# Performance work log

Hardware: AMD Instinct MI355X
Metric: run time of the kernel (lower is better)

## Reference

```python
import jax, jax.numpy as jnp
import numpy as np

D_MODEL = 1024
N_HEADS = 16
HEAD_DIM = D_MODEL // N_HEADS
D_FF = 4096
SEQ = 2048
BATCH = 4
THETA = 10000.0
EPS = 1e-5


def rmsnorm(x, w, eps=EPS):
    xf = x.astype(jnp.float32)
    var = jnp.mean(xf * xf, axis=-1, keepdims=True) + eps
    return (xf * jax.lax.rsqrt(var) * w).astype(x.dtype)


def rope_tables(head_dim, max_len, theta):
    freqs = 1.0 / theta ** (jnp.arange(0, head_dim, 2, dtype=jnp.float32) / head_dim)
    t = jnp.arange(max_len, dtype=jnp.float32)
    ang = jnp.outer(t, freqs)  # [T, Hs/2]
    return jnp.cos(ang), jnp.sin(ang)


def apply_rope(x, cos, sin):
    # x: [B, H, T, Hs]; cos/sin: [T, Hs/2] (broadcast over B, H)
    x1 = x[..., 0::2]
    x2 = x[..., 1::2]
    o1 = x1 * cos - x2 * sin
    o2 = x1 * sin + x2 * cos
    return jnp.stack([o1, o2], axis=-1).reshape(x.shape).astype(x.dtype)


def setup_inputs() -> dict:
    key = jax.random.key(0)
    ks = jax.random.split(key, 12)
    s = 0.02
    return {
        "x": jax.random.normal(ks[0], (BATCH, SEQ, D_MODEL), dtype=jnp.float32),
        "token_positions": jnp.arange(SEQ, dtype=jnp.int32),
        "ln1_w": jnp.ones((D_MODEL,), dtype=jnp.float32),
        "q_w": jax.random.normal(ks[1], (D_MODEL, D_MODEL), dtype=jnp.float32) * s,
        "k_w": jax.random.normal(ks[2], (D_MODEL, D_MODEL), dtype=jnp.float32) * s,
        "v_w": jax.random.normal(ks[3], (D_MODEL, D_MODEL), dtype=jnp.float32) * s,
        "o_w": jax.random.normal(ks[4], (D_MODEL, D_MODEL), dtype=jnp.float32) * s,
        "ln2_w": jnp.ones((D_MODEL,), dtype=jnp.float32),
        "w1": jax.random.normal(ks[5], (D_FF, D_MODEL), dtype=jnp.float32) * s,
        "w2": jax.random.normal(ks[6], (D_MODEL, D_FF), dtype=jnp.float32) * s,
        "w3": jax.random.normal(ks[7], (D_FF, D_MODEL), dtype=jnp.float32) * s,
    }


def reference(x, token_positions, ln1_w, q_w, k_w, v_w, o_w, ln2_w, w1, w2, w3):
    B, T, D = x.shape
    cos_full, sin_full = rope_tables(HEAD_DIM, SEQ, THETA)
    cos = cos_full[token_positions]
    sin = sin_full[token_positions]

    # --- attention sublayer ---
    h = rmsnorm(x, ln1_w)
    q = jnp.einsum('btd,od->bto', h, q_w)
    k = jnp.einsum('btd,od->bto', h, k_w)
    v = jnp.einsum('btd,od->bto', h, v_w)
    # [B, T, D] -> [B, H, T, Hs]
    def split_heads(t_):
        return t_.reshape(B, T, N_HEADS, HEAD_DIM).transpose(0, 2, 1, 3)
    xq, xk, xv = split_heads(q), split_heads(k), split_heads(v)
    xq = apply_rope(xq, cos, sin)
    xk = apply_rope(xk, cos, sin)

    scores = jnp.einsum('bhqd,bhkd->bhqk', xq, xk) / jnp.sqrt(jnp.float32(HEAD_DIM))
    causal = jnp.tril(jnp.ones((T, T), dtype=bool))
    scores = jnp.where(causal, scores, jnp.float32(-jnp.inf))
    attn = jax.nn.softmax(scores, axis=-1)
    ctx = jnp.einsum('bhqk,bhkd->bhqd', attn, xv)
    ctx = ctx.transpose(0, 2, 1, 3).reshape(B, T, D)
    x = x + jnp.einsum('btd,od->bto', ctx, o_w)

    # --- SwiGLU FFN sublayer ---
    h2 = rmsnorm(x, ln2_w)
    a = jnp.einsum('btd,fd->btf', h2, w1)
    g = jnp.einsum('btd,fd->btf', h2, w3)
    ff = jnp.einsum('btf,df->btd', a * jax.nn.sigmoid(a) * g, w2)
    return x + ff
```

## Files before the change

### kernel.cpp

```cpp
#include <hip/hip_runtime.h>
#include <hip/hip_bf16.h>

#define D_MODEL 1024
#define N_HEADS 16
#define HEAD_DIM 64
#define D_FF 4096
#define SEQ 2048
#define BATCH 4
#define NTOK (BATCH*SEQ)
#define QS 3072

typedef __attribute__((ext_vector_type(4))) float  f32x4;
typedef __attribute__((ext_vector_type(8))) short  s16x8;
typedef __attribute__((ext_vector_type(4))) unsigned short u16x4;

typedef __attribute__((address_space(1))) const unsigned int gas_u32;
typedef __attribute__((address_space(3))) unsigned int las_u32;

__device__ __forceinline__ void gload_lds16(const void* g, void* l) {
  __builtin_amdgcn_global_load_lds((gas_u32*)g, (las_u32*)l, 16, 0, 0);
}

__device__ __forceinline__ float bf2f(unsigned short u) {
  union { unsigned int i; float f; } v; v.i = ((unsigned int)u) << 16; return v.f;
}
__device__ __forceinline__ unsigned short f2bf(float f) {
  union { float f; unsigned int i; } v; v.f = f;
  return (unsigned short)((v.i + 0x7fffu + ((v.i >> 16) & 1u)) >> 16);
}

__global__ __launch_bounds__(256) void cvt_all_k(const float* __restrict__ qw, const float* __restrict__ kw,
                                                 const float* __restrict__ vw, const float* __restrict__ ow,
                                                 const float* __restrict__ w1, const float* __restrict__ w2,
                                                 const float* __restrict__ w3,
                                                 unsigned short* __restrict__ wqkv, unsigned short* __restrict__ wo,
                                                 unsigned short* __restrict__ b1, unsigned short* __restrict__ b2,
                                                 unsigned short* __restrict__ b3) {
  const long MM = 1 << 20;
  long e = ((long)blockIdx.x*256 + threadIdx.x)*4;
  const float* src; unsigned short* dst; long off;
  if      (e <    MM) { src = qw; dst = wqkv;        off = e; }
  else if (e <  2*MM) { src = kw; dst = wqkv + MM;   off = e - MM; }
  else if (e <  3*MM) { src = vw; dst = wqkv + 2*MM; off = e - 2*MM; }
  else if (e <  4*MM) { src = ow; dst = wo;          off = e - 3*MM; }
  else if (e <  8*MM) { src = w1; dst = b1;          off = e - 4*MM; }
  else if (e < 12*MM) { src = w2; dst = b2;          off = e - 8*MM; }
  else                { src = w3; dst = b3;          off = e - 12*MM; }
  f32x4 v = *(const f32x4*)&src[off];
  u16x4 o;
  #pragma unroll
  for (int c=0;c<4;c++) o[c] = f2bf(v[c]);
  *(u16x4*)&dst[off] = o;
}

__global__ __launch_bounds__(256) void rope_tables_k(const int* __restrict__ pos,
                                                     float* __restrict__ cosT,
                                                     float* __restrict__ sinT) {
  int idx = blockIdx.x*256 + threadIdx.x;
  int t = idx >> 5, i = idx & 31;
  float p  = (float)pos[t];
  float fr = powf(10000.0f, -(float)i * (1.0f/32.0f));
  float ang = p * fr;
  cosT[idx] = cosf(ang);
  sinT[idx] = sinf(ang);
}

__global__ __launch_bounds__(256) void rmsnorm_k(const float* __restrict__ x,
                                                 const float* __restrict__ wgt,
                                                 unsigned short* __restrict__ out) {
  const long row = blockIdx.x;
  const int t = threadIdx.x;
  f32x4 v = *(const f32x4*)&x[row*D_MODEL + t*4];
  float ss = v[0]*v[0] + v[1]*v[1] + v[2]*v[2] + v[3]*v[3];
  #pragma unroll
  for (int off=1; off<64; off<<=1) ss += __shfl_xor(ss, off, 64);
  __shared__ float red[4];
  if ((t & 63) == 0) red[t >> 6] = ss;
  __syncthreads();
  float tot = red[0] + red[1] + red[2] + red[3];
  float inv = rsqrtf(tot * (1.0f/D_MODEL) + 1e-5f);
  f32x4 wv = *(const f32x4*)&wgt[t*4];
  u16x4 o;
  #pragma unroll
  for (int c=0;c<4;c++) o[c] = f2bf(v[c] * inv * wv[c]);
  *(u16x4*)&out[row*D_MODEL + t*4] = o;
}

__global__ __launch_bounds__(256) void rope_k(unsigned short* __restrict__ qkv,
                                              const float* __restrict__ cosT,
                                              const float* __restrict__ sinT) {
  long idx = (long)blockIdx.x*256 + threadIdx.x;
  int ig = (int)(idx & 7);
  long th = idx >> 3;
  int h = (int)(th & 15);
  long bt = th >> 4;
  int t = (int)(bt & (SEQ-1));
  long off = bt*QS + h*HEAD_DIM + ig*8;
  f32x4 cs = *(const f32x4*)&cosT[t*32 + ig*4];
  f32x4 sn = *(const f32x4*)&sinT[t*32 + ig*4];
  s16x8 qv = *(const s16x8*)&qkv[off];
  s16x8 kv = *(const s16x8*)&qkv[off + 1024];
  s16x8 qo, ko;
  #pragma unroll
  for (int p=0;p<4;p++) {
    float q1 = bf2f((unsigned short)qv[2*p]), q2 = bf2f((unsigned short)qv[2*p+1]);
    qo[2*p]   = (short)f2bf((q1*cs[p] - q2*sn[p]) * 0.125f);
    qo[2*p+1] = (short)f2bf((q1*sn[p] + q2*cs[p]) * 0.125f);
    float k1 = bf2f((unsigned short)kv[2*p]), k2 = bf2f((unsigned short)kv[2*p+1]);
    ko[2*p]   = (short)f2bf(k1*cs[p] - k2*sn[p]);
    ko[2*p+1] = (short)f2bf(k1*sn[p] + k2*cs[p]);
  }
  *(s16x8*)&qkv[off] = qo;
  *(s16x8*)&qkv[off + 1024] = ko;
}

template<int EPI>
__global__ __launch_bounds__(512, 2) void gemm8p(const unsigned short* __restrict__ A,
                                                 const unsigned short* __restrict__ W,
                                                 unsigned short* __restrict__ Cb,
                                                 float* __restrict__ Cf,
                                                 const float* __restrict__ resid,
                                                 int M, int N, int K) {
  __shared__ __align__(16) unsigned short As[3][256*64];
  __shared__ __align__(16) unsigned short Bs[3][128*64];

  const int nwg = gridDim.x * gridDim.y;
  int orig = blockIdx.y * gridDim.x + blockIdx.x;
  int swz = orig;
  if ((nwg & 7) == 0) { int cpx = nwg >> 3; swz = (orig & 7) * cpx + (orig >> 3); }
  const int bx = swz % gridDim.x;
  const int by = swz / gridDim.x;

  const int tid = threadIdx.x;
  const int wid = tid >> 6;
  const int l  = tid & 63;
  const int lr = l & 15;
  const int lg = l >> 4;
  const int wm = (wid >> 2) * 128;
  const int wn = (wid & 3) * 32;

  const long rowA0 = (long)by * 256;
  const long rowB0 = (long)bx * 128;
  const int nk = K >> 6;

  auto stA = [&](int bf, int kt, int it) {
    int chunk = it*512 + tid;
    int row = chunk >> 3;
    int csw = (chunk & 7) ^ (row & 7);
    gload_lds16(&A[(rowA0 + row)*(long)K + kt + csw*8], &As[bf][chunk*8]);
  };
  auto stB = [&](int bf, int kt, int it) {
    int chunk = it*512 + tid;
    int row = chunk >> 3;
    int csw = (chunk & 7) ^ (row & 7);
    gload_lds16(&W[(rowB0 + row)*(long)K + kt + csw*8], &Bs[bf][chunk*8]);
  };

  f32x4 acc[8][2] = {};

  stA(0,0,0); stA(0,0,1); stA(0,0,2); stA(0,0,3); stB(0,0,0); stB(0,0,1);
  stA(1,64,0); stA(1,64,1); stA(1,64,2); stA(1,64,3); stB(1,64,0); stB(1,64,1);
  asm volatile("s_waitcnt vmcnt(6)" ::: "memory");
  __builtin_amdgcn_s_barrier();

  int buf = 0;
  for (int ki = 0; ki < nk; ++ki) {
    const int sb = (buf >= 1) ? buf - 1 : buf + 2;
    const int kt2 = (ki + 2) << 6;
    const bool st = (ki + 2) < nk;

    s16x8 af[2][4], bfr[2][2];
    #pragma unroll
    for (int m=0;m<4;m++) {
      int r = wm + m*16 + lr;
      #pragma unroll
      for (int kk=0;kk<2;kk++)
        af[kk][m] = *(const s16x8*)&As[buf][r*64 + ((kk*4+lg)^(r&7))*8];
    }
    #pragma unroll
    for (int n=0;n<2;n++) {
      int r = wn + n*16 + lr;
      #pragma unroll
      for (int kk=0;kk<2;kk++)
        bfr[kk][n] = *(const s16x8*)&Bs[buf][r*64 + ((kk*4+lg)^(r&7))*8];
    }
    if (st) { stA(sb,kt2,0); stA(sb,kt2,1); stB(sb,kt2,0); }
    __builtin_amdgcn_s_barrier();
    __builtin_amdgcn_s_setprio(1);
    #pragma unroll
    for (int kk=0;kk<2;kk++)
      #pragma unroll
      for (int m=0;m<4;m++)
        #pragma unroll
        for (int n=0;n<2;n++)
          acc[m][n] = __builtin_amdgcn_mfma_f32_16x16x32_bf16(af[kk][m], bfr[kk][n], acc[m][n], 0,0,0);
    __builtin_amdgcn_s_setprio(0);
    __builtin_amdgcn_s_barrier();

    #pragma unroll
    for (int m=0;m<4;m++) {
      int r = wm + 64 + m*16 + lr;
      #pragma unroll
      for (int kk=0;kk<2;kk++)
        af[kk][m] = *(const s16x8*)&As[buf][r*64 + ((kk*4+lg)^(r&7))*8];
    }
    if (st) { stA(sb,kt2,2); stA(sb,kt2,3); stB(sb,kt2,1); }
    __builtin_amdgcn_s_barrier();
    __builtin_amdgcn_s_setprio(1);
    #pragma unroll
    for (int kk=0;kk<2;kk++)
      #pragma unroll
      for (int m=0;m<4;m++)
        #pragma unroll
        for (int n=0;n<2;n++)
          acc[4+m][n] = __builtin_amdgcn_mfma_f32_16x16x32_bf16(af[kk][m], bfr[kk][n], acc[4+m][n], 0,0,0);
    __builtin_amdgcn_s_setprio(0);
    if (st)             { asm volatile("s_waitcnt vmcnt(6)" ::: "memory"); }
    else if (ki+1 < nk) { asm volatile("s_waitcnt vmcnt(0)" ::: "memory"); }
    __builtin_amdgcn_s_barrier();

    buf = (buf == 2) ? 0 : buf + 1;
  }

  #pragma unroll
  for (int mi=0;mi<8;mi++)
    #pragma unroll
    for (int n=0;n<2;n++)
      #pragma unroll
      for (int rr=0;rr<4;rr++) {
        long row = rowA0 + wm + mi*16 + lg*4 + rr;
        long col = rowB0 + wn + n*16 + lr;
        float val = acc[mi][n][rr];
        if constexpr (EPI == 0) {
          Cb[row*(long)N + col] = f2bf(val);
        } else {
          Cf[row*(long)N + col] = resid[row*(long)N + col] + val;
        }
      }
}

__global__ __launch_bounds__(256) void attn_k(const unsigned short* __restrict__ QKV,
                                              unsigned short* __restrict__ O) {
  const int bh = blockIdx.x;
  const int b = bh >> 4;
  const int h = bh & 15;
  const int tid = threadIdx.x;
  const int w  = tid >> 6;
  const int l  = tid & 63;
  const int lr = l & 15;
  const int lg = l >> 4;

  const unsigned short* Qp = QKV;
  const unsigned short* Kp = QKV + 1024;
  const unsigned short* Vp = QKV + 2048;

  __shared__ __align__(16) unsigned short Ks[2][64*64];
  __shared__ __align__(16) unsigned short Vs[2][64*64];
  __shared__ __align__(16) unsigned short Ps[4][16][64];

  const int skv = tid >> 2;
  const int sd0 = (tid & 3) * 16;
  const long hbase = (long)(b*SEQ)*QS + h*HEAD_DIM;

  for (int pass = 0; pass < 2; ++pass) {
    const int qt = pass ? 31 - (int)blockIdx.y : (int)blockIdx.y;
    const int q0 = qt * 64;
    const int ntile = qt + 1;

    const long rowQ = (long)(b*SEQ + q0 + w*16 + lr);
    s16x8 qf0 = *(const s16x8*)&Qp[rowQ*QS + h*HEAD_DIM + lg*8];
    s16x8 qf1 = *(const s16x8*)&Qp[rowQ*QS + h*HEAD_DIM + 32 + lg*8];

    float mi = -1e30f, li = 0.f;
    f32x4 oa[4] = {};

    #pragma unroll
    for (int it=0; it<2; ++it) {
      int chunk = it*256 + tid;
      int row = chunk >> 3;
      int csw = (chunk & 7) ^ (row & 7);
      gload_lds16(&Kp[hbase + (long)row*QS + csw*8], &Ks[0][chunk*8]);
    }
    {
      const unsigned short* src = &Vp[hbase + (long)skv*QS + sd0];
      s16x8 v0 = *(const s16x8*)&src[0];
      s16x8 v1 = *(const s16x8*)&src[8];
      #pragma unroll
      for (int i=0;i<16;i++) {
        int d = sd0 + i;
        int key = (d&7) ^ ((d>>3)&7);
        int c = (skv>>3) ^ key;
        Vs[0][d*64 + c*8 + (skv&7)] = (unsigned short)(i<8 ? v0[i] : v1[i-8]);
      }
    }
    __syncthreads();

    for (int t=0; t<ntile; ++t) {
      const int kv0 = t*64;
      const int cur = t & 1;
      const int nb  = cur ^ 1;
      const bool more = (t+1 < ntile);

      s16x8 v0, v1;
      if (more) {
        #pragma unroll
        for (int it=0; it<2; ++it) {
          int chunk = it*256 + tid;
          int row = chunk >> 3;
          int csw = (chunk & 7) ^ (row & 7);
          gload_lds16(&Kp[hbase + (long)(kv0 + 64 + row)*QS + csw*8], &Ks[nb][chunk*8]);
        }
        const unsigned short* src = &Vp[hbase + (long)(kv0 + 64 + skv)*QS + sd0];
        v0 = *(const s16x8*)&src[0];
        v1 = *(const s16x8*)&src[8];
      }

      f32x4 s[4];
      __builtin_amdgcn_s_setprio(1);
      #pragma unroll
      for (int j=0;j<4;j++) {
        int krow = j*16 + lr;
        s16x8 kf0 = *(const s16x8*)&Ks[cur][krow*64 + ((lg)     ^ (krow&7))*8];
        s16x8 kf1 = *(const s16x8*)&Ks[cur][krow*64 + ((4 + lg) ^ (krow&7))*8];
        f32x4 acc = {};
        acc = __builtin_amdgcn_mfma_f32_16x16x32_bf16(kf0, qf0, acc, 0,0,0);
        acc = __builtin_amdgcn_mfma_f32_16x16x32_bf16(kf1, qf1, acc, 0,0,0);
        s[j] = acc;
      }
      __builtin_amdgcn_s_setprio(0);

      if (t == ntile-1) {
        #pragma unroll
        for (int j=0;j<4;j++)
          #pragma unroll
          for (int r=0;r<4;r++)
            if (kv0 + j*16 + lg*4 + r > q0 + w*16 + lr) s[j][r] = -1e30f;
      }

      float pmax = s[0][0];
      #pragma unroll
      for (int j=0;j<4;j++)
        #pragma unroll
        for (int r=0;r<4;r++) pmax = fmaxf(pmax, s[j][r]);
      pmax = fmaxf(pmax, __shfl_xor(pmax, 16, 64));
      pmax = fmaxf(pmax, __shfl_xor(pmax, 32, 64));
      float mn = fmaxf(mi, pmax);
      float al = __expf(mi - mn);
      mi = mn;
      float psum = 0.f;
      #pragma unroll
      for (int j=0;j<4;j++)
        #pragma unroll
        for (int r=0;r<4;r++) {
          float p = __expf(s[j][r] - mn);
          s[j][r] = p;
          psum += p;
        }
      psum += __shfl_xor(psum, 16, 64);
      psum += __shfl_xor(psum, 32, 64);
      li = li*al + psum;

      float alq[4];
      #pragma unroll
      for (int r=0;r<4;r++) alq[r] = __shfl(al, lg*4 + r, 64);
      #pragma unroll
      for (int d=0;d<4;d++)
        #pragma unroll
        for (int r=0;r<4;r++) oa[d][r] *= alq[r];

      #pragma unroll
      for (int j=0;j<4;j++)
        #pragma unroll
        for (int r=0;r<4;r++) {
          int k = j*16 + lg*4 + r;
          int pos = ((k>>3) ^ (lr&7))*8 + (k&7);
          Ps[w][lr][pos] = f2bf(s[j][r]);
        }

      if (more) {
        #pragma unroll
        for (int i=0;i<16;i++) {
          int d = sd0 + i;
          int key = (d&7) ^ ((d>>3)&7);
          int c = (skv>>3) ^ key;
          Vs[nb][d*64 + c*8 + (skv&7)] = (unsigned short)(i<8 ? v0[i] : v1[i-8]);
        }
      }

      __builtin_amdgcn_s_setprio(1);
      #pragma unroll
      for (int kk=0;kk<2;kk++) {
        s16x8 pa = *(const s16x8*)&Ps[w][lr][((kk*4 + lg) ^ (lr&7))*8];
        #pragma unroll
        for (int d=0;d<4;d++) {
          int vrow = d*16 + lr;
          int key = (vrow&7) ^ ((vrow>>3)&7);
          int c = (kk*4 + lg) ^ key;
          s16x8 vb = *(const s16x8*)&Vs[cur][vrow*64 + c*8];
          oa[d] = __builtin_amdgcn_mfma_f32_16x16x32_bf16(pa, vb, oa[d], 0,0,0);
        }
      }
      __builtin_amdgcn_s_setprio(0);
      __syncthreads();
    }

    float liq[4];
    #pragma unroll
    for (int r=0;r<4;r++) liq[r] = __shfl(li, lg*4 + r, 64);
    #pragma unroll
    for (int d=0;d<4;d++)
      #pragma unroll
      for (int r=0;r<4;r++) {
        long row = (long)(b*SEQ + q0 + w*16 + lg*4 + r);
        O[row*D_MODEL + h*HEAD_DIM + d*16 + lr] = f2bf(oa[d][r] / liq[r]);
      }
  }
}

__global__ __launch_bounds__(256) void swiglu_k(unsigned short* __restrict__ a,
                                                const unsigned short* __restrict__ g) {
  long i = ((long)blockIdx.x*256 + threadIdx.x)*8;
  s16x8 av = *(const s16x8*)&a[i];
  s16x8 gv = *(const s16x8*)&g[i];
  s16x8 o;
  #pragma unroll
  for (int c=0;c<8;c++) {
    float xx = bf2f((unsigned short)av[c]);
    float yy = bf2f((unsigned short)gv[c]);
    float sg = 1.0f / (1.0f + __expf(-xx));
    o[c] = (short)f2bf(xx * sg * yy);
  }
  *(s16x8*)&a[i] = o;
}

extern "C" void kernel_launch(void* const* d_in, const int* in_sizes, int n_in,
                              void* d_out, int out_size, void* d_ws, size_t ws_size,
                              hipStream_t stream) {
  (void)in_sizes; (void)n_in; (void)out_size; (void)ws_size;
  const float* x    = (const float*)d_in[0];
  const int*   tpos = (const int*)d_in[1];
  const float* ln1  = (const float*)d_in[2];
  const float* qw   = (const float*)d_in[3];
  const float* kw   = (const float*)d_in[4];
  const float* vw   = (const float*)d_in[5];
  const float* ow   = (const float*)d_in[6];
  const float* ln2  = (const float*)d_in[7];
  const float* w1   = (const float*)d_in[8];
  const float* w2   = (const float*)d_in[9];
  const float* w3   = (const float*)d_in[10];
  float* out = (float*)d_out;

  char* ws = (char*)d_ws;
  size_t off = 0;
  auto nalloc = [&](size_t b) { void* p = ws + off; off += (b + 255) & ~(size_t)255; return p; };

  unsigned short* wqkvb = (unsigned short*)nalloc((size_t)3072*D_MODEL*2);
  unsigned short* wob   = (unsigned short*)nalloc((size_t)D_MODEL*D_MODEL*2);
  unsigned short* w1b   = (unsigned short*)nalloc((size_t)D_FF*D_MODEL*2);
  unsigned short* w3b   = (unsigned short*)nalloc((size_t)D_FF*D_MODEL*2);
  unsigned short* w2b   = (unsigned short*)nalloc((size_t)D_MODEL*D_FF*2);
  float* cosT = (float*)nalloc((size_t)SEQ*32*4);
  float* sinT = (float*)nalloc((size_t)SEQ*32*4);
  unsigned short* hbuf = (unsigned short*)nalloc((size_t)NTOK*D_MODEL*2);
  unsigned short* qkv  = (unsigned short*)nalloc((size_t)NTOK*QS*2);
  unsigned short* ctxb = (unsigned short*)nalloc((size_t)NTOK*D_MODEL*2);
  float* x2 = (float*)nalloc((size_t)NTOK*D_MODEL*4);
  unsigned short* gbuf = (unsigned short*)nalloc((size_t)NTOK*D_FF*2);
  unsigned short* abuf = qkv;

  cvt_all_k<<<16384,256,0,stream>>>(qw, kw, vw, ow, w1, w2, w3,
                                    wqkvb, wob, w1b, w2b, w3b);
  rope_tables_k<<<SEQ*32/256,256,0,stream>>>(tpos, cosT, sinT);

  rmsnorm_k<<<NTOK,256,0,stream>>>(x, ln1, hbuf);
  gemm8p<0><<<dim3(24,32),512,0,stream>>>(hbuf, wqkvb, qkv, nullptr, nullptr, NTOK, QS, D_MODEL);
  rope_k<<<4096,256,0,stream>>>(qkv, cosT, sinT);
  attn_k<<<dim3(64,16),256,0,stream>>>(qkv, ctxb);
  gemm8p<1><<<dim3(8,32),512,0,stream>>>(ctxb, wob, nullptr, x2, x, NTOK, D_MODEL, D_MODEL);

  rmsnorm_k<<<NTOK,256,0,stream>>>(x2, ln2, hbuf);
  gemm8p<0><<<dim3(32,32),512,0,stream>>>(hbuf, w1b, abuf, nullptr, nullptr, NTOK, D_FF, D_MODEL);
  gemm8p<0><<<dim3(32,32),512,0,stream>>>(hbuf, w3b, gbuf, nullptr, nullptr, NTOK, D_FF, D_MODEL);
  swiglu_k<<<(long)NTOK*D_FF/8/256,256,0,stream>>>(abuf, gbuf);
  gemm8p<1><<<dim3(8,32),512,0,stream>>>(abuf, w2b, nullptr, out, x2, NTOK, D_MODEL, D_FF);
}
```

Measured before the change: 637.8 us.

## Template GEMM on tile shape, use 256x256 tiles with quadrant-split double buffering

The GEMM kernel becomes a template over block and warp tile shape. It switches from a triple-buffered 256x128 pipeline to a double-buffered one that splits each k-step into four MFMA quadrants, with staggered half-tile global-to-LDS loads between them. The QKV and FFN up/gate GEMMs now use 256x256 tiles, which roughly halves operand reloads per output and gives each warp a 128x64 subtile with more MFMA reuse. The cost is more accumulator registers (128 fp32 per thread) at the 2-blocks-per-CU launch bound, LDS use of 128 KB per block, and fewer workgroups for the same GEMMs.

After: 644.5 us. About the same (+1.0%).

```diff
diff --git a/kernel.cpp b/kernel.cpp
--- a/kernel.cpp
+++ b/kernel.cpp
@@ -114,15 +114,24 @@
   *(s16x8*)&qkv[off + 1024] = ko;
 }
 
-template<int EPI>
+template<int EPI, int BM, int BN, int WR, int WC>
 __global__ __launch_bounds__(512, 2) void gemm8p(const unsigned short* __restrict__ A,
                                                  const unsigned short* __restrict__ W,
                                                  unsigned short* __restrict__ Cb,
                                                  float* __restrict__ Cf,
                                                  const float* __restrict__ resid,
                                                  int M, int N, int K) {
-  __shared__ __align__(16) unsigned short As[3][256*64];
-  __shared__ __align__(16) unsigned short Bs[3][128*64];
+  constexpr int WTM = BM / WR;
+  constexpr int WTN = BN / WC;
+  constexpr int MR  = WTM / 16;
+  constexpr int NR  = WTN / 16;
+  constexpr int M2  = MR / 2, N2 = NR / 2;
+  constexpr int LA  = BM / 128;
+  constexpr int LB  = BN / 128;
+  constexpr int VMC = 2*LA + LB;
+
+  __shared__ __align__(16) unsigned short As[2][BM*64];
+  __shared__ __align__(16) unsigned short Bs[2][BN*64];
 
   const int nwg = gridDim.x * gridDim.y;
   int orig = blockIdx.y * gridDim.x + blockIdx.x;
@@ -136,100 +145,104 @@
   const int l  = tid & 63;
   const int lr = l & 15;
   const int lg = l >> 4;
-  const int wm = (wid >> 2) * 128;
-  const int wn = (wid & 3) * 32;
-
-  const long rowA0 = (long)by * 256;
-  const long rowB0 = (long)bx * 128;
+  const int wr = wid / WC;
+  const int wc = wid % WC;
+
+  const long rowA0 = (long)by * BM;
+  const long rowB0 = (long)bx * BN;
   const int nk = K >> 6;
 
-  auto stA = [&](int bf, int kt, int it) {
-    int chunk = it*512 + tid;
-    int row = chunk >> 3;
-    int csw = (chunk & 7) ^ (row & 7);
-    gload_lds16(&A[(rowA0 + row)*(long)K + kt + csw*8], &As[bf][chunk*8]);
+  auto stA = [&](int b, int kt, int h) {
+    #pragma unroll
+    for (int it = 0; it < LA; ++it) {
+      int c = it*512 + tid;
+      int row = h*(BM/2) + (c >> 3);
+      int csw = (c & 7) ^ (row & 7);
+      gload_lds16(&A[(rowA0 + row)*(long)K + kt + csw*8], &As[b][row*64 + (c&7)*8]);
+    }
   };
-  auto stB = [&](int bf, int kt, int it) {
-    int chunk = it*512 + tid;
-    int row = chunk >> 3;
-    int csw = (chunk & 7) ^ (row & 7);
-    gload_lds16(&W[(rowB0 + row)*(long)K + kt + csw*8], &Bs[bf][chunk*8]);
+  auto stB = [&](int b, int kt, int h) {
+    #pragma unroll
+    for (int it = 0; it < LB; ++it) {
+      int c = it*512 + tid;
+      int row = h*(BN/2) + (c >> 3);
+      int csw = (c & 7) ^ (row & 7);
+      gload_lds16(&W[(rowB0 + row)*(long)K + kt + csw*8], &Bs[b][row*64 + (c&7)*8]);
+    }
   };
 
-  f32x4 acc[8][2] = {};
-
-  stA(0,0,0); stA(0,0,1); stA(0,0,2); stA(0,0,3); stB(0,0,0); stB(0,0,1);
-  stA(1,64,0); stA(1,64,1); stA(1,64,2); stA(1,64,3); stB(1,64,0); stB(1,64,1);
-  asm volatile("s_waitcnt vmcnt(6)" ::: "memory");
+  f32x4 acc[MR][NR] = {};
+  s16x8 afr[MR][2], bfr[NR][2];
+
+  auto ldA = [&](int b, int mh) {
+    #pragma unroll
+    for (int m=0;m<M2;m++) {
+      int row = wr*WTM + (mh*M2+m)*16 + lr;
+      #pragma unroll
+      for (int kk=0;kk<2;kk++)
+        afr[mh*M2+m][kk] = *(const s16x8*)&As[b][row*64 + ((kk*4+lg)^(row&7))*8];
+    }
+  };
+  auto ldB = [&](int b, int nh) {
+    #pragma unroll
+    for (int n=0;n<N2;n++) {
+      int row = wc*WTN + (nh*N2+n)*16 + lr;
+      #pragma unroll
+      for (int kk=0;kk<2;kk++)
+        bfr[nh*N2+n][kk] = *(const s16x8*)&Bs[b][row*64 + ((kk*4+lg)^(row&7))*8];
+    }
+  };
+  auto mm = [&](int mh, int nh) {
+    #pragma unroll
+    for (int kk=0;kk<2;kk++)
+      #pragma unroll
+      for (int m=0;m<M2;m++)
+        #pragma unroll
+        for (int n=0;n<N2;n++)
+          acc[mh*M2+m][nh*N2+n] = __builtin_amdgcn_mfma_f32_16x16x32_bf16(
+              afr[mh*M2+m][kk], bfr[nh*N2+n][kk], acc[mh*M2+m][nh*N2+n], 0,0,0);
+  };
+
+  stA(0,0,0); stA(0,0,1); stB(0,0,0); stB(0,0,1);
+  stA(1,64,0); stA(1,64,1); stB(1,64,0);
+  asm volatile("s_waitcnt vmcnt(%0)" :: "n"(VMC) : "memory");
   __builtin_amdgcn_s_barrier();
 
-  int buf = 0;
-  for (int ki = 0; ki < nk; ++ki) {
-    const int sb = (buf >= 1) ? buf - 1 : buf + 2;
-    const int kt2 = (ki + 2) << 6;
-    const bool st = (ki + 2) < nk;
-
-    s16x8 af[2][4], bfr[2][2];
-    #pragma unroll
-    for (int m=0;m<4;m++) {
-      int r = wm + m*16 + lr;
-      #pragma unroll
-      for (int kk=0;kk<2;kk++)
-        af[kk][m] = *(const s16x8*)&As[buf][r*64 + ((kk*4+lg)^(r&7))*8];
-    }
-    #pragma unroll
-    for (int n=0;n<2;n++) {
-      int r = wn + n*16 + lr;
-      #pragma unroll
-      for (int kk=0;kk<2;kk++)
-        bfr[kk][n] = *(const s16x8*)&Bs[buf][r*64 + ((kk*4+lg)^(r&7))*8];
-    }
-    if (st) { stA(sb,kt2,0); stA(sb,kt2,1); stB(sb,kt2,0); }
-    __builtin_amdgcn_s_barrier();
-    __builtin_amdgcn_s_setprio(1);
-    #pragma unroll
-    for (int kk=0;kk<2;kk++)
-      #pragma unroll
-      for (int m=0;m<4;m++)
-        #pragma unroll
-        for (int n=0;n<2;n++)
-          acc[m][n] = __builtin_amdgcn_mfma_f32_16x16x32_bf16(af[kk][m], bfr[kk][n], acc[m][n], 0,0,0);
-    __builtin_amdgcn_s_setprio(0);
-    __builtin_amdgcn_s_barrier();
-
-    #pragma unroll
-    for (int m=0;m<4;m++) {
-      int r = wm + 64 + m*16 + lr;
-      #pragma unroll
-      for (int kk=0;kk<2;kk++)
-        af[kk][m] = *(const s16x8*)&As[buf][r*64 + ((kk*4+lg)^(r&7))*8];
-    }
-    if (st) { stA(sb,kt2,2); stA(sb,kt2,3); stB(sb,kt2,1); }
-    __builtin_amdgcn_s_barrier();
-    __builtin_amdgcn_s_setprio(1);
-    #pragma unroll
-    for (int kk=0;kk<2;kk++)
-      #pragma unroll
-      for (int m=0;m<4;m++)
-        #pragma unroll
-        for (int n=0;n<2;n++)
-          acc[4+m][n] = __builtin_amdgcn_mfma_f32_16x16x32_bf16(af[kk][m], bfr[kk][n], acc[4+m][n], 0,0,0);
-    __builtin_amdgcn_s_setprio(0);
-    if (st)             { asm volatile("s_waitcnt vmcnt(6)" ::: "memory"); }
-    else if (ki+1 < nk) { asm volatile("s_waitcnt vmcnt(0)" ::: "memory"); }
-    __builtin_amdgcn_s_barrier();
-
-    buf = (buf == 2) ? 0 : buf + 1;
+  int ba = 0;
+  for (int t = 0; t < nk; ++t) {
+    const int kt1 = (t+1) << 6, kt2 = (t+2) << 6;
+    const bool s2 = (t+2) < nk;
+    ldA(ba, 0); ldB(ba, 0);
+    if (t+1 < nk) stB(ba^1, kt1, 1);
+    __builtin_amdgcn_s_barrier();
+    __builtin_amdgcn_s_setprio(1); mm(0,0); __builtin_amdgcn_s_setprio(0);
+    __builtin_amdgcn_s_barrier();
+    ldA(ba, 1); ldB(ba, 1);
+    if (s2) stA(ba, kt2, 0);
+    __builtin_amdgcn_s_barrier();
+    __builtin_amdgcn_s_setprio(1); mm(1,0); __builtin_amdgcn_s_setprio(0);
+    __builtin_amdgcn_s_barrier();
+    if (s2) stA(ba, kt2, 1);
+    __builtin_amdgcn_s_barrier();
+    __builtin_amdgcn_s_setprio(1); mm(0,1); __builtin_amdgcn_s_setprio(0);
+    __builtin_amdgcn_s_barrier();
+    if (s2) stB(ba, kt2, 0);
+    __builtin_amdgcn_s_barrier();
+    __builtin_amdgcn_s_setprio(1); mm(1,1); __builtin_amdgcn_s_setprio(0);
+    if (s2)             { asm volatile("s_waitcnt vmcnt(%0)" :: "n"(VMC) : "memory"); }
+    else if (t+1 < nk)  { asm volatile("s_waitcnt vmcnt(0)" ::: "memory"); }
+    __builtin_amdgcn_s_barrier();
+    ba ^= 1;
   }
 
   #pragma unroll
-  for (int mi=0;mi<8;mi++)
-    #pragma unroll
-    for (int n=0;n<2;n++)
+  for (int mi=0;mi<MR;mi++)
+    #pragma unroll
+    for (int n=0;n<NR;n++)
       #pragma unroll
       for (int rr=0;rr<4;rr++) {
-        long row = rowA0 + wm + mi*16 + lg*4 + rr;
-        long col = rowB0 + wn + n*16 + lr;
+        long row = rowA0 + wr*WTM + mi*16 + lg*4 + rr;
+        long col = rowB0 + wc*WTN + n*16 + lr;
         float val = acc[mi][n][rr];
         if constexpr (EPI == 0) {
           Cb[row*(long)N + col] = f2bf(val);
@@ -473,14 +486,14 @@
   rope_tables_k<<<SEQ*32/256,256,0,stream>>>(tpos, cosT, sinT);
 
   rmsnorm_k<<<NTOK,256,0,stream>>>(x, ln1, hbuf);
-  gemm8p<0><<<dim3(24,32),512,0,stream>>>(hbuf, wqkvb, qkv, nullptr, nullptr, NTOK, QS, D_MODEL);
+  gemm8p<0,256,256,2,4><<<dim3(12,32),512,0,stream>>>(hbuf, wqkvb, qkv, nullptr, nullptr, NTOK, QS, D_MODEL);
   rope_k<<<4096,256,0,stream>>>(qkv, cosT, sinT);
   attn_k<<<dim3(64,16),256,0,stream>>>(qkv, ctxb);
-  gemm8p<1><<<dim3(8,32),512,0,stream>>>(ctxb, wob, nullptr, x2, x, NTOK, D_MODEL, D_MODEL);
+  gemm8p<1,256,128,4,2><<<dim3(8,32),512,0,stream>>>(ctxb, wob, nullptr, x2, x, NTOK, D_MODEL, D_MODEL);
 
   rmsnorm_k<<<NTOK,256,0,stream>>>(x2, ln2, hbuf);
-  gemm8p<0><<<dim3(32,32),512,0,stream>>>(hbuf, w1b, abuf, nullptr, nullptr, NTOK, D_FF, D_MODEL);
-  gemm8p<0><<<dim3(32,32),512,0,stream>>>(hbuf, w3b, gbuf, nullptr, nullptr, NTOK, D_FF, D_MODEL);
+  gemm8p<0,256,256,2,4><<<dim3(16,32),512,0,stream>>>(hbuf, w1b, abuf, nullptr, nullptr, NTOK, D_FF, D_MODEL);
+  gemm8p<0,256,256,2,4><<<dim3(16,32),512,0,stream>>>(hbuf, w3b, gbuf, nullptr, nullptr, NTOK, D_FF, D_MODEL);
   swiglu_k<<<(long)NTOK*D_FF/8/256,256,0,stream>>>(abuf, gbuf);
-  gemm8p<1><<<dim3(8,32),512,0,stream>>>(abuf, w2b, nullptr, out, x2, NTOK, D_MODEL, D_FF);
-}
+  gemm8p<1,256,128,4,2><<<dim3(8,32),512,0,stream>>>(abuf, w2b, nullptr, out, x2, NTOK, D_MODEL, D_FF);
+}
```
